# Kernel tuning notes

Measured on AMD Instinct MI355X. Metric: run time of the kernel, lower is better.

The kernel has to match this reference:

```python
import jax, jax.numpy as jnp
import numpy as np

V, BLOCK, D, H, L = 32000, 2048, 768, 12, 4
B, T = 2, 2048
HD = D // H
FF = 4 * D


def setup_inputs() -> dict:
    key = jax.random.key(0)
    ks = jax.random.split(key, 20)
    s = 0.02
    inp = {
        "idx": jax.random.randint(ks[0], (B, T), 0, V),
        "tok_emb": jax.random.normal(ks[1], (V, D), jnp.float32) * s,
        "pos_emb": jax.random.normal(ks[2], (BLOCK, D), jnp.float32) * s,
        # per-layer stacked params (leading dim L); linear weights stored [in, out]
        "ln1_w": jnp.ones((L, D), jnp.float32),
        "ln1_b": jnp.zeros((L, D), jnp.float32),
        "Wqkv": jax.random.normal(ks[3], (L, D, 3 * D), jnp.float32) * s,
        "bqkv": jnp.zeros((L, 3 * D), jnp.float32),
        "Wproj": jax.random.normal(ks[4], (L, D, D), jnp.float32) * s,
        "bproj": jnp.zeros((L, D), jnp.float32),
        "ln2_w": jnp.ones((L, D), jnp.float32),
        "ln2_b": jnp.zeros((L, D), jnp.float32),
        "Wfc": jax.random.normal(ks[5], (L, D, FF), jnp.float32) * s,
        "bfc": jnp.zeros((L, FF), jnp.float32),
        "Wfc2": jax.random.normal(ks[6], (L, FF, D), jnp.float32) * s,
        "bfc2": jnp.zeros((L, D), jnp.float32),
        "lnf_w": jnp.ones((D,), jnp.float32),
        "lnf_b": jnp.zeros((D,), jnp.float32),
    }
    return inp


def _layernorm(x, w, b, eps=1e-5):
    mu = jnp.mean(x, axis=-1, keepdims=True)
    var = jnp.var(x, axis=-1, keepdims=True)
    return (x - mu) * jax.lax.rsqrt(var + eps) * w + b


def _attn(x, Wqkv, bqkv, Wproj, bproj):
    b, t, c = x.shape
    qkv = x @ Wqkv + bqkv  # [B,T,3D]
    q, k, v = jnp.split(qkv, 3, axis=-1)
    q = q.reshape(b, t, H, HD)
    k = k.reshape(b, t, H, HD)
    v = v.reshape(b, t, H, HD)
    scale = 1.0 / np.sqrt(HD)
    att = jnp.einsum("bthd,bshd->bhts", q, k) * scale  # [B,H,T,T]
    causal = jnp.tril(jnp.ones((t, t), bool))
    att = jnp.where(causal[None, None], att, -jnp.inf)
    att = jax.nn.softmax(att, axis=-1)
    out = jnp.einsum("bhts,bshd->bthd", att, v).reshape(b, t, c)
    return out @ Wproj + bproj


def reference(idx, tok_emb, pos_emb, ln1_w, ln1_b, Wqkv, bqkv, Wproj, bproj,
              ln2_w, ln2_b, Wfc, bfc, Wfc2, bfc2, lnf_w, lnf_b):
    t = idx.shape[1]
    x = tok_emb[idx] + pos_emb[:t][None]  # [B,T,D]
    for l in range(L):
        h = _layernorm(x, ln1_w[l], ln1_b[l])
        x = x + _attn(h, Wqkv[l], bqkv[l], Wproj[l], bproj[l])
        h = _layernorm(x, ln2_w[l], ln2_b[l])
        h = jax.nn.gelu(h @ Wfc[l] + bfc[l], approximate=False) @ Wfc2[l] + bfc2[l]
        x = x + h
    x = _layernorm(x, lnf_w, lnf_b)
    return x @ tok_emb.T  # tied head, [B,T,V]
```

## Files before the change

kernel.cpp:

```cpp
#include <hip/hip_runtime.h>
#include <math.h>

#define VOCAB  32000
#define DMODEL 768
#define NHEAD  12
#define NLAYER 4
#define BATCH  2
#define SEQ    2048
#define HEADD  64
#define FFDIM  3072
#define MROWS  (BATCH*SEQ)

typedef __attribute__((ext_vector_type(8))) short bf16x8;
typedef __attribute__((ext_vector_type(4))) float f32x4;

__device__ __forceinline__ unsigned short f2bf(float f) {
    union { float f; unsigned u; } v; v.f = f;
    unsigned r = v.u + 0x7fffu + ((v.u >> 16) & 1u);
    return (unsigned short)(r >> 16);
}

__device__ __forceinline__ void async_lds16(const unsigned short* g, unsigned short* l) {
    __builtin_amdgcn_global_load_lds(
        (const __attribute__((address_space(1))) unsigned int*)(const void*)g,
        (__attribute__((address_space(3))) unsigned int*)(void*)l, 16, 0, 0);
}

__global__ void cvt_bf16_x4(const float* __restrict__ in, unsigned short* __restrict__ out, int n4) {
    int i = blockIdx.x * blockDim.x + threadIdx.x;
    if (i >= n4) return;
    float4 v = ((const float4*)in)[i];
    uint2 o;
    o.x = (unsigned)f2bf(v.x) | ((unsigned)f2bf(v.y) << 16);
    o.y = (unsigned)f2bf(v.z) | ((unsigned)f2bf(v.w) << 16);
    ((uint2*)out)[i] = o;
}

__global__ void transpose_cvt(const float* __restrict__ W, unsigned short* __restrict__ Wt,
                              int Kdim, int Ndim) {
    __shared__ float tile[32][33];
    int l  = blockIdx.z;
    int k0 = blockIdx.x * 32;
    int n0 = blockIdx.y * 32;
    const float* Wl = W + (size_t)l * Kdim * Ndim;
    unsigned short* Wtl = Wt + (size_t)l * Kdim * Ndim;
    int c = threadIdx.x & 31, r = threadIdx.x >> 5;
#pragma unroll
    for (int i = 0; i < 4; i++)
        tile[r + i * 8][c] = Wl[(size_t)(k0 + r + i * 8) * Ndim + n0 + c];
    __syncthreads();
#pragma unroll
    for (int i = 0; i < 4; i++)
        Wtl[(size_t)(n0 + r + i * 8) * Kdim + k0 + c] = f2bf(tile[c][r + i * 8]);
}

__global__ void embed_kernel(const int* __restrict__ idx, const float* __restrict__ tok,
                             const float* __restrict__ pos, float* __restrict__ x) {
    int row = blockIdx.x;
    int t = row & (SEQ - 1);
    int tr = idx[row];
    const float4* ts = (const float4*)(tok + (size_t)tr * DMODEL);
    const float4* ps = (const float4*)(pos + (size_t)t * DMODEL);
    float4* xs = (float4*)(x + (size_t)row * DMODEL);
    int i = threadIdx.x;
    float4 a = ts[i], b = ps[i];
    xs[i] = make_float4(a.x + b.x, a.y + b.y, a.z + b.z, a.w + b.w);
}

__global__ void layernorm_kernel(const float* __restrict__ x, const float* __restrict__ w,
                                 const float* __restrict__ b, unsigned short* __restrict__ out) {
    int row = blockIdx.x;
    const float* xr = x + (size_t)row * DMODEL;
    int t = threadIdx.x;
    float v0 = xr[t], v1 = xr[t + 256], v2 = xr[t + 512];
    float s = v0 + v1 + v2;
    float ss = v0 * v0 + v1 * v1 + v2 * v2;
#pragma unroll
    for (int off = 32; off >= 1; off >>= 1) {
        s  += __shfl_xor(s, off);
        ss += __shfl_xor(ss, off);
    }
    __shared__ float red[8];
    int wave = t >> 6, lane = t & 63;
    if (lane == 0) { red[wave] = s; red[wave + 4] = ss; }
    __syncthreads();
    s  = red[0] + red[1] + red[2] + red[3];
    ss = red[4] + red[5] + red[6] + red[7];
    float mu = s * (1.0f / DMODEL);
    float var = ss * (1.0f / DMODEL) - mu * mu;
    float rs = rsqrtf(var + 1e-5f);
    unsigned short* orow = out + (size_t)row * DMODEL;
    orow[t]       = f2bf((v0 - mu) * rs * w[t]       + b[t]);
    orow[t + 256] = f2bf((v1 - mu) * rs * w[t + 256] + b[t + 256]);
    orow[t + 512] = f2bf((v2 - mu) * rs * w[t + 512] + b[t + 512]);
}

template <bool GELU_, bool RESID_, bool OUTBF16_, bool BIAS_>
__global__ __launch_bounds__(256) void gemm_kernel(
    const unsigned short* __restrict__ A,
    const unsigned short* __restrict__ Bw,
    const float* __restrict__ bias,
    const float* resid,
    float* Cf, unsigned short* Cb,
    int Ndim, int Kdim) {
    const int bm = blockIdx.x * 128;
    const int bn = blockIdx.y * 128;
    __shared__ unsigned short As[128][32];
    __shared__ unsigned short Bs[128][32];
    int tid = threadIdx.x;
    int wave = tid >> 6, lane = tid & 63;
    int wm = (wave >> 1) * 64, wn = (wave & 1) * 64;
    int quad = lane >> 4, ln = lane & 15;
    int srow = lane >> 2;
    int scol = (lane & 3) * 8;
    f32x4 acc[4][4] = {};

    for (int k0 = 0; k0 < Kdim; k0 += 32) {
        __syncthreads();
#pragma unroll
        for (int i = 0; i < 2; i++) {
            int ch = (wave << 1) | i;
            async_lds16(A  + (size_t)(bm + ch * 16 + srow) * Kdim + k0 + scol, &As[ch * 16][0]);
            async_lds16(Bw + (size_t)(bn + ch * 16 + srow) * Kdim + k0 + scol, &Bs[ch * 16][0]);
        }
        __syncthreads();
        bf16x8 af[4], bfr[4];
#pragma unroll
        for (int tm = 0; tm < 4; tm++) af[tm]  = *(const bf16x8*)(&As[wm + tm * 16 + ln][quad * 8]);
#pragma unroll
        for (int tn = 0; tn < 4; tn++) bfr[tn] = *(const bf16x8*)(&Bs[wn + tn * 16 + ln][quad * 8]);
#pragma unroll
        for (int tm = 0; tm < 4; tm++)
#pragma unroll
            for (int tn = 0; tn < 4; tn++)
                acc[tm][tn] = __builtin_amdgcn_mfma_f32_16x16x32_bf16(af[tm], bfr[tn], acc[tm][tn], 0, 0, 0);
    }

#pragma unroll
    for (int tm = 0; tm < 4; tm++)
#pragma unroll
        for (int tn = 0; tn < 4; tn++)
#pragma unroll
            for (int r = 0; r < 4; r++) {
                int row = bm + wm + tm * 16 + quad * 4 + r;
                int col = bn + wn + tn * 16 + ln;
                float c = acc[tm][tn][r];
                if (BIAS_) c += bias[col];
                if (GELU_) c = 0.5f * c * (1.0f + erff(c * 0.70710678118654752f));
                if (RESID_) c += resid[(size_t)row * Ndim + col];
                if (OUTBF16_) Cb[(size_t)row * Ndim + col] = f2bf(c);
                else          Cf[(size_t)row * Ndim + col] = c;
            }
}

__device__ __forceinline__ void stage_Ax(const unsigned short* A, int Kdim, int bm,
                                         unsigned short (*slotA)[64], int half, int ktile,
                                         int w, int lrow, int scol) {
#pragma unroll
    for (int j = 0; j < 2; j++) {
        int row = j * 128 + half * 64 + w * 8;
        const unsigned short* src = A + (size_t)(bm + row + lrow) * Kdim + ktile * 64 + scol;
        async_lds16(src, &slotA[row][0]);
    }
}
__device__ __forceinline__ void stage_Bx(const unsigned short* Bw, int Kdim, int bn,
                                         unsigned short (*slotB)[64], int half, int ktile,
                                         int w, int lrow, int scol) {
#pragma unroll
    for (int j = 0; j < 2; j++) {
        int gb = j * 64 + w * 8;
        int row = (gb >> 5) * 64 + half * 32 + (gb & 31);
        const unsigned short* src = Bw + (size_t)(bn + row + lrow) * Kdim + ktile * 64 + scol;
        async_lds16(src, &slotB[row][0]);
    }
}

#define PHASE(QM, QN, STAGE_STMT, VM_STMT)                                            \
  { bf16x8 af[4][2], bfv[2][2];                                                        \
    const char* Ab = (const char*)&lds[s][0][0][0];                                    \
    const char* Bb = (const char*)&lds[s][1][0][0];                                    \
    _Pragma("unroll") for (int j = 0; j < 4; j++) {                                    \
      int row = wr * 128 + (QM) * 64 + j * 16 + ln;                                    \
      int rs = row * 128, sw = (row & 7) << 4;                                         \
      _Pragma("unroll") for (int ks = 0; ks < 2; ks++)                                 \
        af[j][ks] = *(const bf16x8*)(Ab + rs + ((ks * 64 + quad * 16) ^ sw));          \
    }                                                                                  \
    _Pragma("unroll") for (int jn = 0; jn < 2; jn++) {                                 \
      int row = wc * 64 + (QN) * 32 + jn * 16 + ln;                                    \
      int rs = row * 128, sw = (row & 7) << 4;                                         \
      _Pragma("unroll") for (int ks = 0; ks < 2; ks++)                                 \
        bfv[jn][ks] = *(const bf16x8*)(Bb + rs + ((ks * 64 + quad * 16) ^ sw));        \
    }                                                                                  \
    STAGE_STMT;                                                                        \
    VM_STMT;                                                                           \
    __builtin_amdgcn_s_barrier(); asm volatile("" ::: "memory");                       \
    asm volatile("s_waitcnt lgkmcnt(0)" ::: "memory");                                 \
    __builtin_amdgcn_s_setprio(1);                                                     \
    _Pragma("unroll") for (int j = 0; j < 4; j++)                                      \
    _Pragma("unroll") for (int jn = 0; jn < 2; jn++)                                   \
    _Pragma("unroll") for (int ks = 0; ks < 2; ks++)                                   \
      acc[(QM) * 4 + j][(QN) * 2 + jn] = __builtin_amdgcn_mfma_f32_16x16x32_bf16(      \
          af[j][ks], bfv[jn][ks], acc[(QM) * 4 + j][(QN) * 2 + jn], 0, 0, 0);          \
    __builtin_amdgcn_s_setprio(0);                                                     \
    __builtin_amdgcn_s_barrier(); asm volatile("" ::: "memory"); }

__global__ __launch_bounds__(512, 2) void gemm256_kernel(
    const unsigned short* __restrict__ A,
    const unsigned short* __restrict__ Bw,
    float* __restrict__ Cf, int Ndim, int Kdim) {
    const int bm = blockIdx.x * 256;
    const int bn = blockIdx.y * 256;
    __shared__ unsigned short lds[2][2][256][64];
    int tid = threadIdx.x;
    int w = tid >> 6, lane = tid & 63;
    int wr = w >> 2, wc = w & 3;
    int quad = lane >> 4, ln = lane & 15;
    int lrow = lane >> 3;
    int scol = ((lane & 7) ^ lrow) << 3;
    f32x4 acc[8][4] = {};
    const int NT = Kdim >> 6;

    stage_Ax(A,  Kdim, bm, lds[0][0], 0, 0, w, lrow, scol);
    stage_Bx(Bw, Kdim, bn, lds[0][1], 0, 0, w, lrow, scol);
    stage_Ax(A,  Kdim, bm, lds[0][0], 1, 0, w, lrow, scol);
    stage_Bx(Bw, Kdim, bn, lds[0][1], 1, 0, w, lrow, scol);
    stage_Ax(A,  Kdim, bm, lds[1][0], 0, 1, w, lrow, scol);
    stage_Bx(Bw, Kdim, bn, lds[1][1], 0, 1, w, lrow, scol);
    asm volatile("s_waitcnt vmcnt(8)" ::: "memory");
    __builtin_amdgcn_s_barrier(); asm volatile("" ::: "memory");

    for (int t = 0; t < NT; t++) {
        const int s = t & 1;
        unsigned short (*nA)[64] = lds[s ^ 1][0];
        unsigned short (*nB)[64] = lds[s ^ 1][1];
        unsigned short (*cA)[64] = lds[s][0];
        unsigned short (*cB)[64] = lds[s][1];
        const bool st1 = (t + 1 < NT), st2 = (t + 2 < NT);

        PHASE(0, 0,
              if (st1) stage_Ax(A, Kdim, bm, nA, 1, t + 1, w, lrow, scol),
              if (st1) asm volatile("s_waitcnt vmcnt(6)" ::: "memory"))
        PHASE(0, 1,
              if (st1) stage_Bx(Bw, Kdim, bn, nB, 1, t + 1, w, lrow, scol),
              if (st1) asm volatile("s_waitcnt vmcnt(10)" ::: "memory"))
        PHASE(1, 0,
              if (st2) stage_Ax(A, Kdim, bm, cA, 0, t + 2, w, lrow, scol), )
        PHASE(1, 1,
              if (st2) stage_Bx(Bw, Kdim, bn, cB, 0, t + 2, w, lrow, scol),
              if (st2) { asm volatile("s_waitcnt vmcnt(8)" ::: "memory"); }
              else if (t == NT - 2) { asm volatile("s_waitcnt vmcnt(0)" ::: "memory"); })
    }

#pragma unroll
    for (int mf = 0; mf < 8; mf++)
#pragma unroll
        for (int nf = 0; nf < 4; nf++)
#pragma unroll
            for (int r = 0; r < 4; r++) {
                int row = bm + wr * 128 + mf * 16 + quad * 4 + r;
                int col = bn + wc * 64 + nf * 16 + ln;
                Cf[(size_t)row * Ndim + col] = acc[mf][nf][r];
            }
}

__global__ __launch_bounds__(512, 2) void attn_kernel(const unsigned short* __restrict__ qkv,
                                                      unsigned short* __restrict__ out) {
    int qtile = 15 - blockIdx.x;
    int bh = blockIdx.y;
    int b = bh / NHEAD, h = bh % NHEAD;
    int q0 = qtile * 128;
    const unsigned short* base = qkv + (size_t)b * SEQ * (3 * DMODEL);

    __shared__ unsigned short Qs[128][72];
    __shared__ unsigned short Ks[64][72];
    __shared__ unsigned short Vs[64][72];
    __shared__ unsigned short Ps[128][72];

    int tid = threadIdx.x, wave = tid >> 6, lane = tid & 63;
    int quad = lane >> 4, ln = lane & 15;

    for (int c = tid; c < 1024; c += 512) {
        int r = c >> 3, col = (c & 7) * 8;
        *(bf16x8*)(&Qs[r][col]) =
            *(const bf16x8*)(base + (size_t)(q0 + r) * (3 * DMODEL) + h * HEADD + col);
    }
    __syncthreads();

    bf16x8 qf[2];
#pragma unroll
    for (int ks = 0; ks < 2; ks++)
        qf[ks] = *(const bf16x8*)(&Qs[wave * 16 + ln][ks * 32 + quad * 8]);

    f32x4 o[4] = {};
    float mst[4], lst[4];
#pragma unroll
    for (int i = 0; i < 4; i++) { mst[i] = -3.0e38f; lst[i] = 0.0f; }

    const float scale = 0.125f;
    int nkt = qtile * 2 + 2;

    for (int kt = 0; kt < nkt; kt++) {
        __syncthreads();
        {
            int c = tid;
            int r = c >> 3, col = (c & 7) * 8;
            *(bf16x8*)(&Ks[r][col]) =
                *(const bf16x8*)(base + (size_t)(kt * 64 + r) * (3 * DMODEL) + DMODEL + h * HEADD + col);
            union { bf16x8 v; unsigned short u[8]; } vv;
            vv.v = *(const bf16x8*)(base + (size_t)(kt * 64 + r) * (3 * DMODEL) + 2 * DMODEL + h * HEADD + col);
#pragma unroll
            for (int j = 0; j < 8; j++) Vs[col + j][r] = vv.u[j];
        }
        __syncthreads();

        f32x4 s[4];
#pragma unroll
        for (int tn = 0; tn < 4; tn++) s[tn] = (f32x4){0.f, 0.f, 0.f, 0.f};
        bf16x8 kf[4][2];
#pragma unroll
        for (int tn = 0; tn < 4; tn++)
#pragma unroll
            for (int ks = 0; ks < 2; ks++)
                kf[tn][ks] = *(const bf16x8*)(&Ks[tn * 16 + ln][ks * 32 + quad * 8]);
#pragma unroll
        for (int tn = 0; tn < 4; tn++)
#pragma unroll
            for (int ks = 0; ks < 2; ks++)
                s[tn] = __builtin_amdgcn_mfma_f32_16x16x32_bf16(qf[ks], kf[tn][ks], s[tn], 0, 0, 0);

        if (kt >= qtile * 2) {
#pragma unroll
            for (int tn = 0; tn < 4; tn++)
#pragma unroll
                for (int r = 0; r < 4; r++) {
                    int qi = q0 + wave * 16 + quad * 4 + r;
                    int kj = kt * 64 + tn * 16 + ln;
                    float sv = s[tn][r] * scale;
                    s[tn][r] = (kj > qi) ? -3.0e38f : sv;
                }
        } else {
#pragma unroll
            for (int tn = 0; tn < 4; tn++)
#pragma unroll
                for (int r = 0; r < 4; r++) s[tn][r] *= scale;
        }

#pragma unroll
        for (int r = 0; r < 4; r++) {
            float mx = fmaxf(fmaxf(s[0][r], s[1][r]), fmaxf(s[2][r], s[3][r]));
#pragma unroll
            for (int msk = 1; msk <= 8; msk <<= 1) mx = fmaxf(mx, __shfl_xor(mx, msk));
            float mnew = fmaxf(mst[r], mx);
            float alpha = __expf(mst[r] - mnew);
            mst[r] = mnew;
            float psum = 0.f;
#pragma unroll
            for (int tn = 0; tn < 4; tn++) {
                float p = __expf(s[tn][r] - mnew);
                s[tn][r] = p;
                psum += p;
            }
#pragma unroll
            for (int msk = 1; msk <= 8; msk <<= 1) psum += __shfl_xor(psum, msk);
            lst[r] = lst[r] * alpha + psum;
#pragma unroll
            for (int nd = 0; nd < 4; nd++) o[nd][r] *= alpha;
        }

#pragma unroll
        for (int tn = 0; tn < 4; tn++)
#pragma unroll
            for (int r = 0; r < 4; r++)
                Ps[wave * 16 + quad * 4 + r][tn * 16 + ln] = f2bf(s[tn][r]);

        bf16x8 pf[2], vf[4][2];
#pragma unroll
        for (int ks = 0; ks < 2; ks++)
            pf[ks] = *(const bf16x8*)(&Ps[wave * 16 + ln][ks * 32 + quad * 8]);
#pragma unroll
        for (int nd = 0; nd < 4; nd++)
#pragma unroll
            for (int ks = 0; ks < 2; ks++)
                vf[nd][ks] = *(const bf16x8*)(&Vs[nd * 16 + ln][ks * 32 + quad * 8]);
#pragma unroll
        for (int nd = 0; nd < 4; nd++)
#pragma unroll
            for (int ks = 0; ks < 2; ks++)
                o[nd] = __builtin_amdgcn_mfma_f32_16x16x32_bf16(pf[ks], vf[nd][ks], o[nd], 0, 0, 0);
    }

#pragma unroll
    for (int r = 0; r < 4; r++) {
        float inv = 1.0f / lst[r];
        int trow = q0 + wave * 16 + quad * 4 + r;
#pragma unroll
        for (int nd = 0; nd < 4; nd++) {
            int col = h * HEADD + nd * 16 + ln;
            out[(size_t)(b * SEQ + trow) * DMODEL + col] = f2bf(o[nd][r] * inv);
        }
    }
}

extern "C" void kernel_launch(void* const* d_in, const int* in_sizes, int n_in,
                              void* d_out, int out_size, void* d_ws, size_t ws_size,
                              hipStream_t stream) {
    const int*   idx   = (const int*)  d_in[0];
    const float* tok   = (const float*)d_in[1];
    const float* pos   = (const float*)d_in[2];
    const float* ln1w  = (const float*)d_in[3];
    const float* ln1b  = (const float*)d_in[4];
    const float* Wqkv  = (const float*)d_in[5];
    const float* bqkv  = (const float*)d_in[6];
    const float* Wproj = (const float*)d_in[7];
    const float* bproj = (const float*)d_in[8];
    const float* ln2w  = (const float*)d_in[9];
    const float* ln2b  = (const float*)d_in[10];
    const float* Wfc   = (const float*)d_in[11];
    const float* bfc   = (const float*)d_in[12];
    const float* Wfc2  = (const float*)d_in[13];
    const float* bfc2  = (const float*)d_in[14];
    const float* lnfw  = (const float*)d_in[15];
    const float* lnfb  = (const float*)d_in[16];

    char* ob = (char*)d_out;
    unsigned short* qkvb   = (unsigned short*)(ob + 0);
    float*          x      = (float*)(ob + 18874368);
    unsigned short* ffact  = (unsigned short*)(ob + 31457280);
    unsigned short* attnb  = (unsigned short*)(ob + 56623104);
    unsigned short* WqkvT  = (unsigned short*)(ob + 62914560);
    unsigned short* WprojT = (unsigned short*)(ob + 77070336);
    unsigned short* WfcT   = (unsigned short*)(ob + 81788928);
    unsigned short* Wfc2T  = (unsigned short*)(ob + 100663296);
    unsigned short* tokT   = (unsigned short*)d_ws;
    unsigned short* lnout  = (unsigned short*)((char*)d_ws + 49152000);

    cvt_bf16_x4<<<24000, 256, 0, stream>>>(tok, tokT, VOCAB * DMODEL / 4);
    transpose_cvt<<<dim3(24, 72, NLAYER), 256, 0, stream>>>(Wqkv,  WqkvT,  DMODEL, 3 * DMODEL);
    transpose_cvt<<<dim3(24, 24, NLAYER), 256, 0, stream>>>(Wproj, WprojT, DMODEL, DMODEL);
    transpose_cvt<<<dim3(24, 96, NLAYER), 256, 0, stream>>>(Wfc,   WfcT,   DMODEL, FFDIM);
    transpose_cvt<<<dim3(96, 24, NLAYER), 256, 0, stream>>>(Wfc2,  Wfc2T,  FFDIM,  DMODEL);

    embed_kernel<<<MROWS, 192, 0, stream>>>(idx, tok, pos, x);

    for (int l = 0; l < NLAYER; l++) {
        layernorm_kernel<<<MROWS, 256, 0, stream>>>(x, ln1w + l * DMODEL, ln1b + l * DMODEL, lnout);
        gemm_kernel<false, false, true, true><<<dim3(32, 18), 256, 0, stream>>>(
            lnout, WqkvT + (size_t)l * 3 * DMODEL * DMODEL, bqkv + l * 3 * DMODEL,
            nullptr, nullptr, qkvb, 3 * DMODEL, DMODEL);
        attn_kernel<<<dim3(16, BATCH * NHEAD), 512, 0, stream>>>(qkvb, attnb);
        gemm_kernel<false, true, false, true><<<dim3(32, 6), 256, 0, stream>>>(
            attnb, WprojT + (size_t)l * DMODEL * DMODEL, bproj + l * DMODEL,
            x, x, nullptr, DMODEL, DMODEL);
        layernorm_kernel<<<MROWS, 256, 0, stream>>>(x, ln2w + l * DMODEL, ln2b + l * DMODEL, lnout);
        gemm_kernel<true, false, true, true><<<dim3(32, 24), 256, 0, stream>>>(
            lnout, WfcT + (size_t)l * FFDIM * DMODEL, bfc + l * FFDIM,
            nullptr, nullptr, ffact, FFDIM, DMODEL);
        gemm_kernel<false, true, false, true><<<dim3(32, 6), 256, 0, stream>>>(
            ffact, Wfc2T + (size_t)l * FFDIM * DMODEL, bfc2 + l * DMODEL,
            x, x, nullptr, DMODEL, FFDIM);
    }

    layernorm_kernel<<<MROWS, 256, 0, stream>>>(x, lnfw, lnfb, lnout);
    gemm256_kernel<<<dim3(16, 125), 512, 0, stream>>>(lnout, tokT, (float*)d_out, VOCAB, DMODEL);
}
```

Measured before the change: 2.173 ms.

## Double-buffer LDS in 128x128 GEMM and add XCD-aware block swizzle to 256 GEMM

The generic 128x128 GEMM now keeps two LDS buffers and issues the async global-to-LDS loads for the next K tile before computing the current one, waiting on vmcnt instead of a full sync. The goal is to overlap global load latency with MFMA work. The 256x256 LM-head GEMM also remaps workgroup IDs so that neighbouring tiles land on the same XCD (8 chiplets), which should improve L2 reuse. The remap assumes the block count divides evenly by 8, and the extra LDS buffer doubles shared memory use in the small GEMM.

```diff
diff --git a/kernel.cpp b/kernel.cpp
--- a/kernel.cpp
+++ b/kernel.cpp
@@ -105,8 +105,8 @@
     int Ndim, int Kdim) {
     const int bm = blockIdx.x * 128;
     const int bn = blockIdx.y * 128;
-    __shared__ unsigned short As[128][32];
-    __shared__ unsigned short Bs[128][32];
+    __shared__ unsigned short As[2][128][32];
+    __shared__ unsigned short Bs[2][128][32];
     int tid = threadIdx.x;
     int wave = tid >> 6, lane = tid & 63;
     int wm = (wave >> 1) * 64, wn = (wave & 1) * 64;
@@ -114,27 +114,40 @@
     int srow = lane >> 2;
     int scol = (lane & 3) * 8;
     f32x4 acc[4][4] = {};
-
-    for (int k0 = 0; k0 < Kdim; k0 += 32) {
-        __syncthreads();
-#pragma unroll
-        for (int i = 0; i < 2; i++) {
-            int ch = (wave << 1) | i;
-            async_lds16(A  + (size_t)(bm + ch * 16 + srow) * Kdim + k0 + scol, &As[ch * 16][0]);
-            async_lds16(Bw + (size_t)(bn + ch * 16 + srow) * Kdim + k0 + scol, &Bs[ch * 16][0]);
+    const int NT = Kdim >> 5;
+
+#define GSTAGE(T, BUF)                                                                \
+    _Pragma("unroll") for (int i_ = 0; i_ < 2; i_++) {                                \
+        int ch_ = (wave << 1) | i_;                                                   \
+        async_lds16(A  + (size_t)(bm + ch_ * 16 + srow) * Kdim + (T) * 32 + scol,     \
+                    &As[BUF][ch_ * 16][0]);                                           \
+        async_lds16(Bw + (size_t)(bn + ch_ * 16 + srow) * Kdim + (T) * 32 + scol,     \
+                    &Bs[BUF][ch_ * 16][0]);                                           \
+    }
+
+    GSTAGE(0, 0)
+    for (int t = 0; t < NT; t++) {
+        const int cur = t & 1;
+        if (t + 1 < NT) {
+            GSTAGE(t + 1, cur ^ 1)
+            asm volatile("s_waitcnt vmcnt(4)" ::: "memory");
+        } else {
+            asm volatile("s_waitcnt vmcnt(0)" ::: "memory");
         }
-        __syncthreads();
+        __builtin_amdgcn_s_barrier(); asm volatile("" ::: "memory");
         bf16x8 af[4], bfr[4];
 #pragma unroll
-        for (int tm = 0; tm < 4; tm++) af[tm]  = *(const bf16x8*)(&As[wm + tm * 16 + ln][quad * 8]);
-#pragma unroll
-        for (int tn = 0; tn < 4; tn++) bfr[tn] = *(const bf16x8*)(&Bs[wn + tn * 16 + ln][quad * 8]);
+        for (int tm = 0; tm < 4; tm++) af[tm]  = *(const bf16x8*)(&As[cur][wm + tm * 16 + ln][quad * 8]);
+#pragma unroll
+        for (int tn = 0; tn < 4; tn++) bfr[tn] = *(const bf16x8*)(&Bs[cur][wn + tn * 16 + ln][quad * 8]);
 #pragma unroll
         for (int tm = 0; tm < 4; tm++)
 #pragma unroll
             for (int tn = 0; tn < 4; tn++)
                 acc[tm][tn] = __builtin_amdgcn_mfma_f32_16x16x32_bf16(af[tm], bfr[tn], acc[tm][tn], 0, 0, 0);
-    }
+        __builtin_amdgcn_s_barrier(); asm volatile("" ::: "memory");
+    }
+#undef GSTAGE
 
 #pragma unroll
     for (int tm = 0; tm < 4; tm++)
@@ -208,8 +221,12 @@
     const unsigned short* __restrict__ A,
     const unsigned short* __restrict__ Bw,
     float* __restrict__ Cf, int Ndim, int Kdim) {
-    const int bm = blockIdx.x * 256;
-    const int bn = blockIdx.y * 256;
+    int lin = blockIdx.x + (int)gridDim.x * blockIdx.y;
+    int nwg = (int)gridDim.x * (int)gridDim.y;
+    int cpx = nwg >> 3;
+    int swz = (lin & 7) * cpx + (lin >> 3);
+    const int bm = (swz % (int)gridDim.x) * 256;
+    const int bn = (swz / (int)gridDim.x) * 256;
     __shared__ unsigned short lds[2][2][256][64];
     int tid = threadIdx.x;
     int w = tid >> 6, lane = tid & 63;
```

Result: faster. 2.103 ms (-3.2%).
